# Kernel optimization log

Measured on AMD Instinct MI355X. Metric: run time of the kernel, lower is better.

Reference implementation:

```python
import jax, jax.numpy as jnp
import numpy as np

B, S, E = 2, 1024, 1024
H, DH = 16, 64           # num_heads, key_dim = E // H
MAXLEN = 2048            # config.max_sequence_length -> table size 2*MAXLEN-1


def setup_inputs() -> dict:
    key = jax.random.key(0)
    ks = jax.random.split(key, 13)
    sc = 1.0 / np.sqrt(E)
    return {
        "query": jax.random.normal(ks[0], (B, S, E), jnp.float32),
        "key": jax.random.normal(ks[1], (B, S, E), jnp.float32),
        "value": jax.random.normal(ks[2], (B, S, E), jnp.float32),
        "Wq": jax.random.normal(ks[3], (E, E), jnp.float32) * sc,
        "bq": jnp.zeros((E,), jnp.float32),
        "Wk": jax.random.normal(ks[4], (E, E), jnp.float32) * sc,
        "bk": jnp.zeros((E,), jnp.float32),
        "Wv": jax.random.normal(ks[5], (E, E), jnp.float32) * sc,
        "bv": jnp.zeros((E,), jnp.float32),
        "Wo": jax.random.normal(ks[6], (E, E), jnp.float32) * sc,
        "bo": jnp.zeros((E,), jnp.float32),
        "rel_pos_emb": jax.random.normal(ks[7], (2 * MAXLEN - 1, DH), jnp.float32) * 0.02,
        "rel_pos_bias": jnp.zeros((2 * MAXLEN - 1,), jnp.float32),
    }


def _split_heads(x):
    # [B, S, E] -> [B, H, S, DH]
    return x.reshape(B, S, H, DH).transpose(0, 2, 1, 3)


def _relative_shift(x):
    # x: [B, H, S, S]; pad one zero column on the left of the last dim,
    # reshape to [B, H, S+1, S], drop the first row -> [B, H, S, S]
    x = jnp.pad(x, ((0, 0), (0, 0), (0, 0), (1, 0)))
    x = x.reshape(B, H, S + 1, S)
    return x[:, :, 1:, :]


def reference(query, key, value, Wq, bq, Wk, bk, Wv, bv, Wo, bo,
              rel_pos_emb, rel_pos_bias):
    q = _split_heads(query @ Wq + bq) / jnp.sqrt(jnp.float32(DH))  # [B,H,S,DH]
    k = _split_heads(key @ Wk + bk)                                 # [B,H,S,DH]
    v = _split_heads(value @ Wv + bv)                               # [B,H,S,DH]

    scores = jnp.einsum("bhid,bhjd->bhij", q, k)  # [B,H,S,S]

    # relative position term (gather + skew, as in the original call())
    pos_ids = jnp.arange(S)[:, None] - jnp.arange(S)[None, :] + (MAXLEN - 1)  # [S,S]
    rpe = rel_pos_emb[pos_ids]    # [S, S, DH]
    rpb = rel_pos_bias[pos_ids]   # [S, S]
    rel = jnp.einsum("bhid,ijd->bhij", q, rpe)  # [B,H,S,S]
    rel = _relative_shift(rel)
    scores = scores + rel + rpb   # rpb broadcasts over [B,H]

    weights = jax.nn.softmax(scores, axis=-1)
    out = jnp.einsum("bhij,bhjd->bhid", weights, v)  # [B,H,S,DH]
    out = out.transpose(0, 2, 1, 3).reshape(B, S, E)
    return out @ Wo + bo
```

## Files before the change

kernel.cpp:

```cpp
#include <hip/hip_runtime.h>

typedef unsigned short u16;
typedef __bf16 bf16_t;
typedef bf16_t bf16x8 __attribute__((ext_vector_type(8)));
typedef u16 u16x8 __attribute__((ext_vector_type(8)));
typedef float f32x4 __attribute__((ext_vector_type(4)));

#define DEVI __device__ __forceinline__


DEVI u16 f2bf(float f) {
    unsigned u = __builtin_bit_cast(unsigned, f);
    u = (u + 0x7FFFu + ((u >> 16) & 1u)) >> 16;
    return (u16)u;
}
DEVI float bf2f(u16 b) {
    unsigned u = ((unsigned)b) << 16;
    return __builtin_bit_cast(float, u);
}
DEVI f32x4 mfma16(u16x8 a, u16x8 b, f32x4 c) {
    return __builtin_amdgcn_mfma_f32_16x16x32_bf16(
        __builtin_bit_cast(bf16x8, a), __builtin_bit_cast(bf16x8, b), c, 0, 0, 0);
}
DEVI void gl2lds(const u16* g, u16* l) {
    __builtin_amdgcn_global_load_lds(
        (__attribute__((address_space(1))) void*)g,
        (__attribute__((address_space(3))) void*)l, 16, 0, 0);
}

__global__ __launch_bounds__(256) void cvt_kernel(
    const float* __restrict__ q, const float* __restrict__ k, const float* __restrict__ v,
    const float* __restrict__ emb,
    u16* __restrict__ xq, u16* __restrict__ xk, u16* __restrict__ xv, u16* __restrict__ embb)
{
    const long NQ = 2097152;
    const long NE = 262080;
    long i4 = ((long)blockIdx.x * 256 + threadIdx.x) * 4;
    if (i4 < 3 * NQ) {
        int which = (int)(i4 >> 21);
        long off = i4 & (NQ - 1);
        const float* src = which == 0 ? q : (which == 1 ? k : v);
        u16* dst = which == 0 ? xq : (which == 1 ? xk : xv);
        float4 f = *(const float4*)(src + off);
        ushort4 o; o.x = f2bf(f.x); o.y = f2bf(f.y); o.z = f2bf(f.z); o.w = f2bf(f.w);
        *(ushort4*)(dst + off) = o;
    } else {
        long off = i4 - 3 * NQ;
        if (off < NE) {
            float4 f = *(const float4*)(emb + off);
            ushort4 o; o.x = f2bf(f.x); o.y = f2bf(f.y); o.z = f2bf(f.z); o.w = f2bf(f.w);
            *(ushort4*)(embb + off) = o;
        }
    }
}

__global__ __launch_bounds__(256) void wt_kernel(
    const float* __restrict__ w0, const float* __restrict__ w1,
    const float* __restrict__ w2, const float* __restrict__ w3,
    u16* __restrict__ t0, u16* __restrict__ t1, u16* __restrict__ t2, u16* __restrict__ t3)
{
    int z = blockIdx.z;
    const float* W = z == 0 ? w0 : (z == 1 ? w1 : (z == 2 ? w2 : w3));
    u16* T = z == 0 ? t0 : (z == 1 ? t1 : (z == 2 ? t2 : t3));
    __shared__ float tile[64][65];
    int k0 = blockIdx.y * 64, n0 = blockIdx.x * 64;
    int tx = threadIdx.x, ty = threadIdx.y;
    for (int r = ty; r < 64; r += 4)
        tile[r][tx] = W[(long)(k0 + r) * 1024 + n0 + tx];
    __syncthreads();
    for (int r = ty; r < 64; r += 4)
        T[(long)(n0 + r) * 1024 + k0 + tx] = f2bf(tile[tx][r]);
}

template<int MT>
__global__ __launch_bounds__(256) void gemm_kernel(
    const u16* __restrict__ A0, const u16* __restrict__ A1, const u16* __restrict__ A2,
    const u16* __restrict__ W0, const u16* __restrict__ W1, const u16* __restrict__ W2,
    const float* __restrict__ bias0, const float* __restrict__ bias1, const float* __restrict__ bias2,
    u16* __restrict__ o0, u16* __restrict__ o1, u16* __restrict__ o2,
    float* __restrict__ ofp, int mode_base)
{
    int z = blockIdx.z;
    int mode = mode_base + z;
    const u16* A = z == 0 ? A0 : (z == 1 ? A1 : A2);
    const u16* W = z == 0 ? W0 : (z == 1 ? W1 : W2);
    const float* bias = z == 0 ? bias0 : (z == 1 ? bias1 : bias2);
    u16* ob = z == 0 ? o0 : (z == 1 ? o1 : o2);

    constexpr int MROWS = MT * 32;
    __shared__ u16 la[2 * MROWS * 32];
    __shared__ u16 lw[2 * 128 * 32];

    int lin = blockIdx.x + (blockIdx.y << 3);
    int xcd = lin & 7, idx = lin >> 3;
    int xt = (xcd & 1) * 4 + (idx & 3);
    int yt = (xcd >> 1) * 8 + (idx >> 2);
    int m0 = yt * MROWS, n0 = xt * 128;

    int t = threadIdx.x, lane = t & 63, wid = t >> 6;
    int l15 = lane & 15, quad = lane >> 4;
    int wm = (wid >> 1) * (MT * 16), wn = (wid & 1) * 64;
    int sr = lane >> 2, sp = lane & 3;

    f32x4 acc[MT][4] = {};

    auto stage = [&](int buf, int k0) {
#pragma unroll
        for (int q = 0; q < MT / 2; q++) {
            int r = wid * (MT * 8) + q * 16 + sr;
            int c = sp ^ ((r >> 1) & 3);
            gl2lds(A + (long)(m0 + r) * 1024 + k0 + c * 8,
                   la + buf * (MROWS * 32) + (wid * (MT * 8) + q * 16) * 32);
        }
#pragma unroll
        for (int q = 0; q < 2; q++) {
            int r = wid * 32 + q * 16 + sr;
            int c = sp ^ ((r >> 1) & 3);
            gl2lds(W + (long)(n0 + r) * 1024 + k0 + c * 8,
                   lw + buf * (128 * 32) + (wid * 32 + q * 16) * 32);
        }
    };

    stage(0, 0);
    __syncthreads();
    int cur = 0;
#pragma unroll 1
    for (int k0 = 0; k0 < 1024; k0 += 32) {
        if (k0 < 992) stage(cur ^ 1, k0 + 32);
        const u16* lab = la + cur * (MROWS * 32);
        const u16* lwb = lw + cur * (128 * 32);
        u16x8 af[MT], bfr[4];
#pragma unroll
        for (int mt = 0; mt < MT; mt++) {
            int r = wm + mt * 16 + l15;
            af[mt] = *(const u16x8*)&lab[r * 32 + ((quad ^ ((r >> 1) & 3)) * 8)];
        }
#pragma unroll
        for (int nt = 0; nt < 4; nt++) {
            int r = wn + nt * 16 + l15;
            bfr[nt] = *(const u16x8*)&lwb[r * 32 + ((quad ^ ((r >> 1) & 3)) * 8)];
        }
#pragma unroll
        for (int mt = 0; mt < MT; mt++)
#pragma unroll
            for (int nt = 0; nt < 4; nt++)
                acc[mt][nt] = mfma16(af[mt], bfr[nt], acc[mt][nt]);
        __syncthreads();
        cur ^= 1;
    }

#pragma unroll
    for (int mt = 0; mt < MT; mt++)
#pragma unroll
        for (int nt = 0; nt < 4; nt++)
#pragma unroll
            for (int reg = 0; reg < 4; reg++) {
                int gm = m0 + wm + mt * 16 + quad * 4 + reg;
                int gn = n0 + wn + nt * 16 + l15;
                float val = acc[mt][nt][reg] + bias[gn];
                if (mode == 0) {
                    val *= 0.125f;
                    long o = ((long)((gm >> 10) * 16 + (gn >> 6)) << 16) + ((gm & 1023) << 6) + (gn & 63);
                    ob[o] = f2bf(val);
                } else if (mode == 1) {
                    long o = ((long)((gm >> 10) * 16 + (gn >> 6)) << 16) + ((gm & 1023) << 6) + (gn & 63);
                    ob[o] = f2bf(val);
                } else if (mode == 2) {
                    long o = ((long)((gm >> 10) * 16 + (gn >> 6)) << 16) + ((long)(gn & 63) << 10) + (gm & 1023);
                    ob[o] = f2bf(val);
                } else {
                    ofp[(long)gm * 1024 + gn] = val;
                }
            }
}

__global__ __launch_bounds__(256) void gc_kernel(
    const u16* __restrict__ qb, const u16* __restrict__ embb,
    const float* __restrict__ rpb, u16* __restrict__ Bskew)
{
    int u0 = blockIdx.x * 16;
    int i0 = u0 & 1023;
    int t = threadIdx.x, lane = t & 63, wid = t >> 6;
    int l15 = lane & 15, quad = lane >> 4;

    __shared__ u16 lds_s[16][1032];

    u16x8 aq[2];
    long qoff = (long)(u0 + l15) * 64 + quad * 8;
    aq[0] = *(const u16x8*)&qb[qoff];
    aq[1] = *(const u16x8*)&qb[qoff + 32];

    for (int tt = wid; tt < 65; tt += 4) {
        int w0 = tt * 16;
        long ebase = (long)(1024 + i0 + w0 + l15) * 64 + quad * 8;
        u16x8 b0 = *(const u16x8*)&embb[ebase];
        u16x8 b1 = *(const u16x8*)&embb[ebase + 32];
        f32x4 c = {};
        c = mfma16(aq[0], b0, c);
        c = mfma16(aq[1], b1, c);
#pragma unroll
        for (int reg = 0; reg < 4; reg++) {
            int r = quad * 4 + reg;
            int cc = w0 + l15 - r;
            if ((unsigned)cc <= 1023u) {
                int i = i0 + r;
                float rb = rpb[cc + (cc <= i ? 2047 : 1022)];
                lds_s[r][cc] = f2bf(c[reg] + rb);
            }
        }
    }
    __syncthreads();
#pragma unroll
    for (int rd = 0; rd < 8; rd++) {
        int r = rd * 2 + (t >> 7);
        int ch = t & 127;
        u16x8 vv = *(const u16x8*)&lds_s[r][ch * 8];
        *(u16x8*)&Bskew[((long)(u0 + r) << 10) + ch * 8] = vv;
    }
}

__global__ __launch_bounds__(256, 4) void flash_kernel(
    const u16* __restrict__ qb, const u16* __restrict__ kb, const u16* __restrict__ vT,
    const u16* __restrict__ Bskew, const float* __restrict__ rpb,
    float* __restrict__ Po, float* __restrict__ Pm, float* __restrict__ Pl)
{
    int itile = blockIdx.x;
    int bh = blockIdx.y;
    int js = blockIdx.z;
    int t = threadIdx.x, lane = t & 63, wid = t >> 6;
    int l15 = lane & 15, quad = lane >> 4;
    int i0w = itile * 64 + wid * 16;

    __shared__ u16 lds_k[64 * 64];
    __shared__ u16 lds_v[64 * 64];
    __shared__ u16 lds_p[4][16][72];

    int sr8 = lane >> 3, sp8 = lane & 7;

    float rpb2046 = rpb[2046];

    u16x8 aq[2];
    {
        long qoff = ((long)(bh * 1024) + i0w + l15) * 64 + quad * 8;
        aq[0] = *(const u16x8*)&qb[qoff];
        aq[1] = *(const u16x8*)&qb[qoff + 32];
    }
    float m_r[4], l_r[4];
    f32x4 o_acc[4] = {};
#pragma unroll
    for (int r = 0; r < 4; r++) { m_r[r] = -1e30f; l_r[r] = 0.f; }

    const u16* kbase = kb + (long)bh * 65536;
    const u16* vbase = vT + (long)bh * 65536;
    const u16* bbase = Bskew + ((long)bh << 20);

    for (int jt = 0; jt < 8; jt++) {
        int j0 = js * 512 + jt * 64;
        __syncthreads();
#pragma unroll
        for (int q = 0; q < 2; q++) {
            int r = wid * 16 + q * 8 + sr8;
            int c = sp8 ^ (r & 7);
            gl2lds(kbase + (long)(j0 + r) * 64 + c * 8, lds_k + (wid * 16 + q * 8) * 64);
            gl2lds(vbase + (long)r * 1024 + j0 + c * 8, lds_v + (wid * 16 + q * 8) * 64);
        }
        __syncthreads();

        f32x4 s_acc[4];
#pragma unroll
        for (int nt = 0; nt < 4; nt++) {
            int r = nt * 16 + l15;
            u16x8 b0 = *(const u16x8*)&lds_k[r * 64 + ((quad ^ (r & 7)) * 8)];
            u16x8 b1 = *(const u16x8*)&lds_k[r * 64 + (((quad + 4) ^ (r & 7)) * 8)];
            f32x4 c = {};
            c = mfma16(aq[0], b0, c);
            c = mfma16(aq[1], b1, c);
            s_acc[nt] = c;
        }

#pragma unroll
        for (int nt = 0; nt < 4; nt++) {
            int jn0 = j0 + nt * 16;
            int jj = jn0 + l15;
            if (jn0 + 15 <= i0w) {
#pragma unroll
                for (int reg = 0; reg < 4; reg++) {
                    int ii = i0w + quad * 4 + reg;
                    s_acc[nt][reg] += bf2f(bbase[((long)ii << 10) + (ii - jj)]);
                }
            } else if (jn0 >= i0w + 17) {
#pragma unroll
                for (int reg = 0; reg < 4; reg++) {
                    int ii = i0w + quad * 4 + reg;
                    s_acc[nt][reg] += bf2f(bbase[((long)(ii + 1) << 10) + (ii + 1025 - jj)]);
                }
            } else {
#pragma unroll
                for (int reg = 0; reg < 4; reg++) {
                    int ii = i0w + quad * 4 + reg;
                    float a;
                    if (jj <= ii)          a = bf2f(bbase[((long)ii << 10) + (ii - jj)]);
                    else if (jj == ii + 1) a = rpb2046;
                    else                   a = bf2f(bbase[((long)(ii + 1) << 10) + (ii + 1025 - jj)]);
                    s_acc[nt][reg] += a;
                }
            }
        }

#pragma unroll
        for (int reg = 0; reg < 4; reg++) {
            float mx = fmaxf(fmaxf(s_acc[0][reg], s_acc[1][reg]), fmaxf(s_acc[2][reg], s_acc[3][reg]));
            for (int off = 1; off < 16; off <<= 1) mx = fmaxf(mx, __shfl_xor(mx, off, 64));
            float mnew = fmaxf(m_r[reg], mx);
            float alpha = __expf(m_r[reg] - mnew);
            float rs = 0.f;
#pragma unroll
            for (int nt = 0; nt < 4; nt++) {
                float p = __expf(s_acc[nt][reg] - mnew);
                s_acc[nt][reg] = p;
                rs += p;
            }
            for (int off = 1; off < 16; off <<= 1) rs += __shfl_xor(rs, off, 64);
            l_r[reg] = l_r[reg] * alpha + rs;
            m_r[reg] = mnew;
#pragma unroll
            for (int dt = 0; dt < 4; dt++) o_acc[dt][reg] *= alpha;
        }

#pragma unroll
        for (int nt = 0; nt < 4; nt++)
#pragma unroll
            for (int reg = 0; reg < 4; reg++)
                lds_p[wid][quad * 4 + reg][nt * 16 + l15] = f2bf(s_acc[nt][reg]);

        u16x8 pf0 = *(const u16x8*)&lds_p[wid][l15][quad * 8];
        u16x8 pf1 = *(const u16x8*)&lds_p[wid][l15][quad * 8 + 32];
#pragma unroll
        for (int dt = 0; dt < 4; dt++) {
            int r = dt * 16 + l15;
            u16x8 v0 = *(const u16x8*)&lds_v[r * 64 + ((quad ^ (r & 7)) * 8)];
            u16x8 v1 = *(const u16x8*)&lds_v[r * 64 + (((quad + 4) ^ (r & 7)) * 8)];
            o_acc[dt] = mfma16(pf0, v0, o_acc[dt]);
            o_acc[dt] = mfma16(pf1, v1, o_acc[dt]);
        }
    }

    int blk = (js * 32 + bh) * 16 + itile;
    float* PoB = Po + (long)blk * 4096;
#pragma unroll
    for (int dt = 0; dt < 4; dt++)
#pragma unroll
        for (int reg = 0; reg < 4; reg++) {
            int rr = wid * 16 + quad * 4 + reg;
            PoB[rr * 64 + dt * 16 + l15] = o_acc[dt][reg];
        }
    if (l15 == 0) {
#pragma unroll
        for (int reg = 0; reg < 4; reg++) {
            int rr = wid * 16 + quad * 4 + reg;
            Pm[blk * 64 + rr] = m_r[reg];
            Pl[blk * 64 + rr] = l_r[reg];
        }
    }
}

__global__ __launch_bounds__(256) void combine_kernel(
    const float* __restrict__ Po, const float* __restrict__ Pm, const float* __restrict__ Pl,
    u16* __restrict__ attn)
{
    int itile = blockIdx.x, bh = blockIdx.y;
    int t = threadIdx.x;
    int c = t & 63, rg = t >> 6;
    int blk0 = bh * 16 + itile;
    int blk1 = (32 + bh) * 16 + itile;
    int b = bh >> 4, h = bh & 15;
    for (int rr = rg; rr < 64; rr += 4) {
        float m0 = Pm[blk0 * 64 + rr], m1 = Pm[blk1 * 64 + rr];
        float ms = fmaxf(m0, m1);
        float e0 = __expf(m0 - ms), e1 = __expf(m1 - ms);
        float l = Pl[blk0 * 64 + rr] * e0 + Pl[blk1 * 64 + rr] * e1;
        float o = Po[(long)blk0 * 4096 + rr * 64 + c] * e0
                + Po[(long)blk1 * 4096 + rr * 64 + c] * e1;
        int ii = itile * 64 + rr;
        attn[((long)(b * 1024 + ii)) * 1024 + h * 64 + c] = f2bf(o / l);
    }
}

extern "C" void kernel_launch(void* const* d_in, const int* in_sizes, int n_in,
                              void* d_out, int out_size, void* d_ws, size_t ws_size,
                              hipStream_t stream)
{
    const float* query = (const float*)d_in[0];
    const float* key_  = (const float*)d_in[1];
    const float* value = (const float*)d_in[2];
    const float* Wq = (const float*)d_in[3];
    const float* bq = (const float*)d_in[4];
    const float* Wk = (const float*)d_in[5];
    const float* bk = (const float*)d_in[6];
    const float* Wv = (const float*)d_in[7];
    const float* bv = (const float*)d_in[8];
    const float* Wo = (const float*)d_in[9];
    const float* bo = (const float*)d_in[10];
    const float* emb = (const float*)d_in[11];
    const float* rpb = (const float*)d_in[12];

    char* ws = (char*)d_ws;
    u16* xq   = (u16*)(ws + 0);
    u16* xk   = (u16*)(ws + 4194304);
    u16* xv   = (u16*)(ws + 8388608);
    u16* WqT  = (u16*)(ws + 12582912);
    u16* WkT  = (u16*)(ws + 14680064);
    u16* WvT  = (u16*)(ws + 16777216);
    u16* embb = (u16*)(ws + 18874368);
    u16* WoT  = (u16*)(ws + 19922944);
    u16* qb   = (u16*)(ws + 22020096);
    u16* kb   = (u16*)(ws + 26214400);
    u16* vT   = (u16*)(ws + 30408704);
    u16* Bskew= (u16*)(ws + 34603008);
    float* Po = (float*)(ws + 0);
    float* Pm = (float*)(ws + 16777216);
    float* Pl = (float*)(ws + 17039360);
    u16* attn = (u16*)(ws + 22020096);

    cvt_kernel<<<6400, 256, 0, stream>>>(query, key_, value, emb, xq, xk, xv, embb);
    wt_kernel<<<dim3(16, 16, 4), dim3(64, 4), 0, stream>>>(Wq, Wk, Wv, Wo, WqT, WkT, WvT, WoT);
    gemm_kernel<2><<<dim3(8, 32, 3), 256, 0, stream>>>(xq, xk, xv, WqT, WkT, WvT,
                                                       bq, bk, bv, qb, kb, vT, nullptr, 0);
    gc_kernel<<<2048, 256, 0, stream>>>(qb, embb, rpb, Bskew);
    flash_kernel<<<dim3(16, 32, 2), 256, 0, stream>>>(qb, kb, vT, Bskew, rpb, Po, Pm, Pl);
    combine_kernel<<<dim3(16, 32), 256, 0, stream>>>(Po, Pm, Pl, attn);
    gemm_kernel<2><<<dim3(8, 32, 1), 256, 0, stream>>>(attn, nullptr, nullptr, WoT, nullptr, nullptr,
                                                       bo, nullptr, nullptr,
                                                       nullptr, nullptr, nullptr, (float*)d_out, 3);
}
```

Before: 260.2 us.

## Process 32 rows per block in relative-position kernel, reuse embedding loads

The relative-position score kernel now handles 32 query rows per block instead of 16. Each loaded embedding tile feeds two row groups of MFMAs, which halves the block count and the embedding traffic per row. Embedding loads are software-prefetched one iteration ahead, and the bias lookup reads a copy of the needed part of the bias table staged in LDS. The LDS staging of the output tile is removed, so results go straight to global memory as scattered 2-byte stores, which risks poorly coalesced writes.

```diff
diff --git a/kernel.cpp b/kernel.cpp
--- a/kernel.cpp
+++ b/kernel.cpp
@@ -178,44 +178,57 @@
     const u16* __restrict__ qb, const u16* __restrict__ embb,
     const float* __restrict__ rpb, u16* __restrict__ Bskew)
 {
-    int u0 = blockIdx.x * 16;
+    int u0 = blockIdx.x * 32;
     int i0 = u0 & 1023;
     int t = threadIdx.x, lane = t & 63, wid = t >> 6;
     int l15 = lane & 15, quad = lane >> 4;
 
-    __shared__ u16 lds_s[16][1032];
-
-    u16x8 aq[2];
-    long qoff = (long)(u0 + l15) * 64 + quad * 8;
-    aq[0] = *(const u16x8*)&qb[qoff];
-    aq[1] = *(const u16x8*)&qb[qoff + 32];
-
-    for (int tt = wid; tt < 65; tt += 4) {
+    __shared__ float lds_rpb[2048];
+    for (int j = t; j < 1024; j += 256) {
+        lds_rpb[j] = rpb[j + 2047];
+        lds_rpb[1024 + j] = rpb[j + 1022];
+    }
+    __syncthreads();
+
+    u16x8 aq[2][2];
+#pragma unroll
+    for (int rg = 0; rg < 2; rg++) {
+        long qoff = (long)(u0 + rg * 16 + l15) * 64 + quad * 8;
+        aq[rg][0] = *(const u16x8*)&qb[qoff];
+        aq[rg][1] = *(const u16x8*)&qb[qoff + 32];
+    }
+
+    u16x8 nb0, nb1;
+    {
+        long ebase = (long)(1024 + i0 + wid * 16 + l15) * 64 + quad * 8;
+        nb0 = *(const u16x8*)&embb[ebase];
+        nb1 = *(const u16x8*)&embb[ebase + 32];
+    }
+
+    for (int tt = wid; tt < 66; tt += 4) {
+        u16x8 b0 = nb0, b1 = nb1;
+        if (tt + 4 < 66) {
+            long ebase = (long)(1024 + i0 + (tt + 4) * 16 + l15) * 64 + quad * 8;
+            nb0 = *(const u16x8*)&embb[ebase];
+            nb1 = *(const u16x8*)&embb[ebase + 32];
+        }
         int w0 = tt * 16;
-        long ebase = (long)(1024 + i0 + w0 + l15) * 64 + quad * 8;
-        u16x8 b0 = *(const u16x8*)&embb[ebase];
-        u16x8 b1 = *(const u16x8*)&embb[ebase + 32];
-        f32x4 c = {};
-        c = mfma16(aq[0], b0, c);
-        c = mfma16(aq[1], b1, c);
-#pragma unroll
-        for (int reg = 0; reg < 4; reg++) {
-            int r = quad * 4 + reg;
-            int cc = w0 + l15 - r;
-            if ((unsigned)cc <= 1023u) {
-                int i = i0 + r;
-                float rb = rpb[cc + (cc <= i ? 2047 : 1022)];
-                lds_s[r][cc] = f2bf(c[reg] + rb);
+#pragma unroll
+        for (int rg = 0; rg < 2; rg++) {
+            f32x4 c = {};
+            c = mfma16(aq[rg][0], b0, c);
+            c = mfma16(aq[rg][1], b1, c);
+#pragma unroll
+            for (int reg = 0; reg < 4; reg++) {
+                int row = rg * 16 + quad * 4 + reg;
+                int cc = w0 + l15 - row;
+                if ((unsigned)cc <= 1023u) {
+                    int i = i0 + row;
+                    float rb = lds_rpb[cc + ((cc <= i) ? 0 : 1024)];
+                    Bskew[((long)(u0 + row) << 10) + cc] = f2bf(c[reg] + rb);
+                }
             }
         }
-    }
-    __syncthreads();
-#pragma unroll
-    for (int rd = 0; rd < 8; rd++) {
-        int r = rd * 2 + (t >> 7);
-        int ch = t & 127;
-        u16x8 vv = *(const u16x8*)&lds_s[r][ch * 8];
-        *(u16x8*)&Bskew[((long)(u0 + r) << 10) + ch * 8] = vv;
     }
 }
 
@@ -426,7 +439,7 @@
     wt_kernel<<<dim3(16, 16, 4), dim3(64, 4), 0, stream>>>(Wq, Wk, Wv, Wo, WqT, WkT, WvT, WoT);
     gemm_kernel<2><<<dim3(8, 32, 3), 256, 0, stream>>>(xq, xk, xv, WqT, WkT, WvT,
                                                        bq, bk, bv, qb, kb, vT, nullptr, 0);
-    gc_kernel<<<2048, 256, 0, stream>>>(qb, embb, rpb, Bskew);
+    gc_kernel<<<1024, 256, 0, stream>>>(qb, embb, rpb, Bskew);
     flash_kernel<<<dim3(16, 32, 2), 256, 0, stream>>>(qb, kb, vT, Bskew, rpb, Po, Pm, Pl);
     combine_kernel<<<dim3(16, 32), 256, 0, stream>>>(Po, Pm, Pl, attn);
     gemm_kernel<2><<<dim3(8, 32, 1), 256, 0, stream>>>(attn, nullptr, nullptr, WoT, nullptr, nullptr,
```

New measurement: 240.1 us. 7.7% less time.
